# Kernel optimization log

Hardware: AMD Instinct MI355X
Metric: run time of the kernel (lower is better)

Reference implementation:

```python
import jax, jax.numpy as jnp
import numpy as np

DIM = 128
N_CENTERS = 30
CUT_LO, CUT_HI = 0.0, 10.0
N_CONV = 3
NODE_VOCAB = 100
EDGE_VOCAB = 500
N_NODES = 50000
N_EDGES = 800000
N_GRAPHS = 100
DIM_E = DIM + N_CENTERS  # 158


def setup_inputs() -> dict:
    key = jax.random.key(0)
    ks = jax.random.split(key, 20)
    def xav(k, shape):
        fan_in = shape[-2] if len(shape) >= 2 else shape[-1]
        return (jax.random.normal(k, shape, dtype=jnp.float32) / np.sqrt(fan_in)).astype(jnp.float32)
    inp = {
        'node_types': jax.random.randint(ks[0], (N_NODES,), 0, NODE_VOCAB),
        'edge_types': jax.random.randint(ks[1], (N_EDGES,), 0, EDGE_VOCAB),
        'src': jax.random.randint(ks[2], (N_EDGES,), 0, N_NODES),
        'dst': jax.random.randint(ks[3], (N_EDGES,), 0, N_NODES),
        'graph_ids': jnp.sort(jax.random.randint(ks[4], (N_NODES,), 0, N_GRAPHS)),
        'distances': jax.random.uniform(ks[5], (N_EDGES,), dtype=jnp.float32, minval=CUT_LO, maxval=CUT_HI),
        'n_graphs': N_GRAPHS,
        # embedding tables
        'node_emb': xav(ks[6], (NODE_VOCAB, DIM)),
        'edge_emb': xav(ks[7], (EDGE_VOCAB, DIM)),
        # stacked per-conv-layer weights (n_conv leading dim)
        'Wn1': xav(ks[8], (N_CONV, DIM, DIM)),  'bn1': jnp.zeros((N_CONV, DIM), jnp.float32),
        'Wn2': xav(ks[9], (N_CONV, DIM, DIM)),  'bn2': jnp.zeros((N_CONV, DIM), jnp.float32),
        'We1': xav(ks[10], (N_CONV, DIM_E, DIM)), 'be1': jnp.zeros((N_CONV, DIM), jnp.float32),
        'We2': xav(ks[11], (N_CONV, DIM, DIM)),  'be2': jnp.zeros((N_CONV, DIM), jnp.float32),
        'Wc':  xav(ks[12], (N_CONV, DIM, DIM)),  'bc': jnp.zeros((N_CONV, DIM), jnp.float32),
        # read layer
        'Wr1': xav(ks[13], (DIM, DIM)), 'br1': jnp.zeros((DIM,), jnp.float32),
        'Wr2': xav(ks[14], (DIM, 1)),   'br2': jnp.zeros((1,), jnp.float32),
    }
    return inp


def reference(node_types, edge_types, src, dst, graph_ids, distances, n_graphs,
              node_emb, edge_emb, Wn1, bn1, Wn2, bn2, We1, be1, We2, be2, Wc, bc,
              Wr1, br1, Wr2, br2):
    # embeddings
    h = node_emb[node_types]                      # [N, D]
    e_emb = edge_emb[edge_types]                  # [E, D]
    # RBF expansion of distances
    centers = jnp.linspace(CUT_LO, CUT_HI, N_CENTERS, dtype=jnp.float32)
    gap = centers[1] - centers[0]
    rbf = jnp.exp(-((distances[:, None] - centers[None, :]) ** 2) / gap)  # [E, n_centers]
    e = jnp.concatenate([e_emb, rbf], axis=1)     # [E, D + n_centers]

    n_nodes = h.shape[0]
    for i in range(N_CONV):
        node_path = jnp.maximum(h[src] @ Wn1[i] + bn1[i], 0.0) @ Wn2[i] + bn2[i]   # [E, D]
        edge_path = jnp.maximum(e @ We1[i] + be1[i], 0.0) @ We2[i] + be2[i]        # [E, D]
        m = jnp.tanh((node_path * edge_path) @ Wc[i] + bc[i])                       # [E, D]
        h = h + jax.ops.segment_sum(m, dst, num_segments=n_nodes)                   # scatter-add to dst

    # readout MLP + per-graph node sum
    hr = jnp.maximum(h @ Wr1 + br1, 0.0) @ Wr2 + br2                                # [N, 1]
    out = jax.ops.segment_sum(hr, graph_ids, num_segments=n_graphs)                 # [G, 1]
    return out.reshape(-1)
```

## Files before the change

### kernel.cpp

```cpp
#include <hip/hip_runtime.h>
#include <stdint.h>

#define NNODES 50000
#define NEDGES 800000
#define NGRAPH 100
#define NTILES (NEDGES / 128)

typedef _Float16 f16;
typedef __attribute__((ext_vector_type(8))) _Float16 half8;
typedef __attribute__((ext_vector_type(4))) float floatx4;

__device__ __forceinline__ void stage_WT(const float* __restrict__ W, f16* WT,
                                         int tid, int nthr) {
    for (int idx = tid; idx < 128 * 32; idx += nthr) {
        int k = idx >> 5, n4 = (idx & 31) * 4;
        floatx4 v = *(const floatx4*)(W + k * 128 + n4);
        WT[(n4 + 0) * 136 + k] = (f16)v[0];
        WT[(n4 + 1) * 136 + k] = (f16)v[1];
        WT[(n4 + 2) * 136 + k] = (f16)v[2];
        WT[(n4 + 3) * 136 + k] = (f16)v[3];
    }
}

__device__ __forceinline__ float fast_tanh(float x) {
    x = fminf(fmaxf(x, -15.0f), 15.0f);
    float e2 = __expf(2.0f * x);
    return (e2 - 1.0f) * __builtin_amdgcn_rcpf(e2 + 1.0f);
}

__global__ void init_k(float* out, int osz, int* cnt) {
    int i = blockIdx.x * 256 + threadIdx.x;
    if (i < osz) out[i] = 0.0f;
    if (i < NNODES) cnt[i] = 0;
}

__global__ void hist_k(const int* __restrict__ dst, int* __restrict__ cnt) {
    int e = blockIdx.x * 256 + threadIdx.x;
    if (e < NEDGES) atomicAdd(&cnt[dst[e]], 1);
}

__global__ __launch_bounds__(1024) void scan1_k(const int* __restrict__ cnt,
                                                int* __restrict__ rowStart,
                                                int* __restrict__ blockSum) {
    __shared__ int buf[1024];
    int tid = threadIdx.x;
    int i = blockIdx.x * 1024 + tid;
    int v = (i < NNODES) ? cnt[i] : 0;
    buf[tid] = v;
    __syncthreads();
    for (int off = 1; off < 1024; off <<= 1) {
        int t = (tid >= off) ? buf[tid - off] : 0;
        __syncthreads();
        buf[tid] += t;
        __syncthreads();
    }
    if (i < NNODES) rowStart[i] = buf[tid] - v;
    if (tid == 1023) blockSum[blockIdx.x] = buf[1023];
}

__global__ void scan2_k(int* __restrict__ blockSum, int nb) {
    if (threadIdx.x == 0) {
        int run = 0;
        for (int b = 0; b < nb; ++b) { int s = blockSum[b]; blockSum[b] = run; run += s; }
    }
}

__global__ __launch_bounds__(1024) void scan3_k(int* __restrict__ rowStart,
                                                const int* __restrict__ blockSum,
                                                int* __restrict__ cnt) {
    int i = blockIdx.x * 1024 + threadIdx.x;
    if (i < NNODES) { rowStart[i] += blockSum[blockIdx.x]; cnt[i] = 0; }
    if (i == 0) rowStart[NNODES] = NEDGES;
}

__global__ void scatter_k(const int* __restrict__ src, const int* __restrict__ et,
                          const int* __restrict__ dst, const float* __restrict__ dist,
                          const int* __restrict__ rowStart, int* __restrict__ cnt,
                          uint4* __restrict__ packE) {
    int e = blockIdx.x * 256 + threadIdx.x;
    if (e >= NEDGES) return;
    int d = dst[e];
    int pos = rowStart[d] + atomicAdd(&cnt[d], 1);
    uint4 pk;
    pk.x = (unsigned)src[e];
    pk.y = (unsigned)et[e];
    pk.z = (unsigned)d;
    pk.w = __float_as_uint(dist[e]);
    packE[pos] = pk;
}

__global__ void gather_h(const int* __restrict__ nt, const float* __restrict__ emb,
                         float* __restrict__ h) {
    int i = blockIdx.x * 256 + threadIdx.x;
    int row = i >> 5, c4 = (i & 31) * 4;
    if (row < NNODES)
        *(floatx4*)(h + row * 128 + c4) = *(const floatx4*)(emb + nt[row] * 128 + c4);
}

template <int MODE>
__global__ __launch_bounds__(1024, 4) void mlp_kernel(
        const float* __restrict__ X, int M,
        const float* __restrict__ W1, const float* __restrict__ b1,
        const float* __restrict__ W2, const float* __restrict__ b2,
        f16* __restrict__ Out) {
    __shared__ f16 W1T[128 * 136];
    __shared__ f16 W2T[(MODE == 0) ? 128 * 136 : 8];
    __shared__ f16 xBuf[256 * 136];
    __shared__ float bias1[128];
    __shared__ float bias2[128];
    int tid = threadIdx.x;

    stage_WT(W1, W1T, tid, 1024);
    if (MODE == 0) stage_WT(W2, W2T, tid, 1024);
    if (tid < 128) { bias1[tid] = b1[tid]; bias2[tid] = (MODE == 0) ? b2[tid] : 0.0f; }

    int r0 = blockIdx.x * 256;
    for (int it = 0; it < 8; ++it) {
        int row = it * 32 + (tid >> 5);
        int c4 = (tid & 31) * 4;
        int gr = r0 + row;
        floatx4 x = {0.0f, 0.0f, 0.0f, 0.0f};
        if (gr < M) x = *(const floatx4*)(X + (size_t)gr * 128 + c4);
        f16* dph = xBuf + row * 136 + c4;
        dph[0] = (f16)x[0]; dph[1] = (f16)x[1]; dph[2] = (f16)x[2]; dph[3] = (f16)x[3];
    }
    __syncthreads();

    int lane = tid & 63, wv = tid >> 6;
    int R = wv * 16;
    int n16 = lane & 15, q = lane >> 4;

    half8 a[4];
    #pragma unroll
    for (int kk = 0; kk < 4; ++kk)
        a[kk] = *(const half8*)(xBuf + (R + n16) * 136 + kk * 32 + q * 8);

    floatx4 acc[8];
    #pragma unroll
    for (int f = 0; f < 8; ++f) {
        float bb = bias1[f * 16 + n16];
        acc[f] = (floatx4){bb, bb, bb, bb};
        #pragma unroll
        for (int kk = 0; kk < 4; ++kk) {
            half8 b = *(const half8*)(W1T + (f * 16 + n16) * 136 + kk * 32 + q * 8);
            acc[f] = __builtin_amdgcn_mfma_f32_16x16x32_f16(a[kk], b, acc[f], 0, 0, 0);
        }
    }

    if (MODE == 0) {
        #pragma unroll
        for (int f = 0; f < 8; ++f)
            #pragma unroll
            for (int i = 0; i < 4; ++i)
                xBuf[(R + q * 4 + i) * 136 + f * 16 + n16] = (f16)fmaxf(acc[f][i], 0.0f);
        #pragma unroll
        for (int kk = 0; kk < 4; ++kk)
            a[kk] = *(const half8*)(xBuf + (R + n16) * 136 + kk * 32 + q * 8);
        #pragma unroll
        for (int f = 0; f < 8; ++f) {
            float bb = bias2[f * 16 + n16];
            acc[f] = (floatx4){bb, bb, bb, bb};
            #pragma unroll
            for (int kk = 0; kk < 4; ++kk) {
                half8 b = *(const half8*)(W2T + (f * 16 + n16) * 136 + kk * 32 + q * 8);
                acc[f] = __builtin_amdgcn_mfma_f32_16x16x32_f16(a[kk], b, acc[f], 0, 0, 0);
            }
        }
        #pragma unroll
        for (int f = 0; f < 8; ++f)
            #pragma unroll
            for (int i = 0; i < 4; ++i) {
                int gr = r0 + R + q * 4 + i;
                if (gr < M) Out[(size_t)gr * 128 + f * 16 + n16] = (f16)acc[f][i];
            }
    } else {
        #pragma unroll
        for (int f = 0; f < 8; ++f)
            #pragma unroll
            for (int i = 0; i < 4; ++i) {
                int gr = r0 + R + q * 4 + i;
                float v = acc[f][i];
                if (MODE == 1) v = fmaxf(v, 0.0f);
                if (gr < M) Out[(size_t)gr * 128 + f * 16 + n16] = (f16)v;
            }
    }
}

__global__ __launch_bounds__(1024, 4) void edge_kernel(
        const uint4* __restrict__ packE,
        const f16* __restrict__ P, const f16* __restrict__ T,
        const float* __restrict__ We1,
        const float* __restrict__ We2, const float* __restrict__ be2,
        const float* __restrict__ Wc,  const float* __restrict__ bc,
        float* __restrict__ h) {
    __shared__ f16 W2T[128 * 136];
    __shared__ f16 WcT[128 * 136];
    __shared__ f16 W1rT[128 * 40];
    __shared__ f16 uBuf[2][128 * 136];
    __shared__ float sbe2[128], sbc[128];
    __shared__ int   dstSeg[2][128];
    __shared__ int   srcS[2][128];
    __shared__ float distS[2][128];

    int tid = threadIdx.x;
    stage_WT(We2, W2T, tid, 1024);
    stage_WT(Wc,  WcT, tid, 1024);
    for (int idx = tid; idx < 128 * 32; idx += 1024) {
        int n = idx >> 5, kr = idx & 31;
        W1rT[n * 40 + kr] = (kr < 30) ? (f16)We1[(128 + kr) * 128 + n] : (f16)0.0f;
    }
    if (tid < 128) { sbe2[tid] = be2[tid]; sbc[tid] = bc[tid]; }
    __syncthreads();

    int g = tid >> 9;
    int t = tid & 511;
    int lane = tid & 63, wvg = t >> 6;
    int R = wvg * 16;
    int n16 = lane & 15, q = lane >> 4;
    const float invgap = 29.0f / 10.0f;
    f16* U = uBuf[g];

    int gid = blockIdx.x * 2 + g;
    int blkTiles = (NTILES - blockIdx.x * 2 + 511) / 512;

    for (int it = 0; it < blkTiles; ++it) {
        int tile = gid + it * 512;
        bool active = tile < NTILES;

        if (active) {
            int row = t >> 2, sub = t & 3;
            uint4 pk = packE[(size_t)tile * 128 + row];
            if (sub == 0) {
                dstSeg[g][row] = (int)pk.z;
                srcS[g][row]   = (int)pk.x;
                distS[g][row]  = __uint_as_float(pk.w);
            }
            const uint4* Tp = (const uint4*)(T + (size_t)pk.y * 128 + sub * 32);
            uint4* ub = (uint4*)(U + row * 136 + sub * 32);
            ub[0] = Tp[0]; ub[1] = Tp[1]; ub[2] = Tp[2]; ub[3] = Tp[3];
        }

        {
            float d = distS[g][R + n16];
            half8 ar;
            #pragma unroll
            for (int j = 0; j < 8; ++j) {
                int k = q * 8 + j;
                float c = (float)k * (10.0f / 29.0f);
                float df = d - c;
                ar[j] = (f16)((k < 30) ? __expf(-df * df * invgap) : 0.0f);
            }
            #pragma unroll
            for (int f = 0; f < 8; ++f) {
                int col = f * 16 + n16;
                floatx4 c4;
                #pragma unroll
                for (int i = 0; i < 4; ++i) c4[i] = (float)U[(R + q * 4 + i) * 136 + col];
                half8 br = *(const half8*)(W1rT + col * 40 + q * 8);
                c4 = __builtin_amdgcn_mfma_f32_16x16x32_f16(ar, br, c4, 0, 0, 0);
                #pragma unroll
                for (int i = 0; i < 4; ++i)
                    U[(R + q * 4 + i) * 136 + col] = (f16)fmaxf(c4[i], 0.0f);
            }
        }

        half8 pA[4];
        {
            int srow = active ? srcS[g][R + n16] : 0;
            const f16* Pr = P + (size_t)srow * 128 + q * 8;
            #pragma unroll
            for (int kk = 0; kk < 4; ++kk) pA[kk] = *(const half8*)(Pr + kk * 32);
        }

        half8 a2[4];
        #pragma unroll
        for (int kk = 0; kk < 4; ++kk)
            a2[kk] = *(const half8*)(U + (R + n16) * 136 + kk * 32 + q * 8);
        floatx4 ep[8];
        #pragma unroll
        for (int f = 0; f < 8; ++f) {
            float bb = sbe2[f * 16 + n16];
            ep[f] = (floatx4){bb, bb, bb, bb};
            #pragma unroll
            for (int kk = 0; kk < 4; ++kk) {
                half8 b = *(const half8*)(W2T + (f * 16 + n16) * 136 + kk * 32 + q * 8);
                ep[f] = __builtin_amdgcn_mfma_f32_16x16x32_f16(a2[kk], b, ep[f], 0, 0, 0);
            }
        }

        #pragma unroll
        for (int f = 0; f < 8; ++f) {
            int col = f * 16 + n16;
            #pragma unroll
            for (int i = 0; i < 4; ++i)
                U[(R + q * 4 + i) * 136 + col] = (f16)ep[f][i];
        }

        #pragma unroll
        for (int kk = 0; kk < 4; ++kk) {
            half8 pe = *(const half8*)(U + (R + n16) * 136 + kk * 32 + q * 8);
            a2[kk] = pe * pA[kk];
        }
        floatx4 mm[8];
        #pragma unroll
        for (int f = 0; f < 8; ++f) {
            float bb = sbc[f * 16 + n16];
            mm[f] = (floatx4){bb, bb, bb, bb};
            #pragma unroll
            for (int kk = 0; kk < 4; ++kk) {
                half8 b = *(const half8*)(WcT + (f * 16 + n16) * 136 + kk * 32 + q * 8);
                mm[f] = __builtin_amdgcn_mfma_f32_16x16x32_f16(a2[kk], b, mm[f], 0, 0, 0);
            }
        }
        #pragma unroll
        for (int f = 0; f < 8; ++f)
            #pragma unroll
            for (int i = 0; i < 4; ++i)
                U[(R + q * 4 + i) * 136 + f * 16 + n16] = (f16)fast_tanh(mm[f][i]);
        __syncthreads();

        if (active) {
            int col = t & 127, chunk = t >> 7;
            int rbeg = chunk * 32;
            float acc = 0.0f;
            int prev = dstSeg[g][rbeg];
            for (int r = rbeg; r < rbeg + 32; ++r) {
                int dd = dstSeg[g][r];
                float v = (float)U[r * 136 + col];
                if (dd != prev) {
                    unsafeAtomicAdd(&h[(size_t)prev * 128 + col], acc);
                    acc = v; prev = dd;
                } else acc += v;
            }
            unsafeAtomicAdd(&h[(size_t)prev * 128 + col], acc);
        }
        __syncthreads();
    }
}

__global__ void dot_k(const f16* __restrict__ tbuf, const float* __restrict__ Wr2,
                      const float* __restrict__ br2, const int* __restrict__ gid,
                      float* __restrict__ out) {
    __shared__ float sa[256];
    __shared__ int sg[256];
    int t = threadIdx.x;
    int n = blockIdx.x * 256 + t;
    float acc = 0.0f;
    int g = -1;
    if (n < NNODES) {
        const half8* tp = (const half8*)(tbuf + (size_t)n * 128);
        for (int m = 0; m < 16; ++m) {
            half8 v = tp[m];
            for (int j = 0; j < 8; ++j) acc += (float)v[j] * Wr2[m * 8 + j];
        }
        acc += br2[0];
        g = gid[n];
    }
    sa[t] = acc; sg[t] = g;
    __syncthreads();
    if (n < NNODES) {
        bool head = (t == 0) || (sg[t - 1] != g);
        if (head) {
            float s = 0.0f;
            int r = t;
            while (r < 256 && sg[r] == g) { s += sa[r]; ++r; }
            unsafeAtomicAdd(&out[g], s);
        }
    }
}

extern "C" void kernel_launch(void* const* d_in, const int* in_sizes, int n_in,
                              void* d_out, int out_size, void* d_ws, size_t ws_size,
                              hipStream_t stream) {
    (void)in_sizes; (void)n_in; (void)ws_size;
    const int*   node_types = (const int*)d_in[0];
    const int*   edge_types = (const int*)d_in[1];
    const int*   src        = (const int*)d_in[2];
    const int*   dst        = (const int*)d_in[3];
    const int*   graph_ids  = (const int*)d_in[4];
    const float* distances  = (const float*)d_in[5];
    const float* node_emb   = (const float*)d_in[7];
    const float* edge_emb   = (const float*)d_in[8];
    const float* Wn1 = (const float*)d_in[9];
    const float* bn1 = (const float*)d_in[10];
    const float* Wn2 = (const float*)d_in[11];
    const float* bn2 = (const float*)d_in[12];
    const float* We1 = (const float*)d_in[13];
    const float* be1 = (const float*)d_in[14];
    const float* We2 = (const float*)d_in[15];
    const float* be2 = (const float*)d_in[16];
    const float* Wc  = (const float*)d_in[17];
    const float* bc  = (const float*)d_in[18];
    const float* Wr1 = (const float*)d_in[19];
    const float* br1 = (const float*)d_in[20];
    const float* Wr2 = (const float*)d_in[21];
    const float* br2 = (const float*)d_in[22];

    char* w = (char*)d_ws;
    auto carve = [&](size_t bytes) { char* p = w; w += (bytes + 255) & ~(size_t)255; return p; };
    float* h        = (float*)carve((size_t)NNODES * 128 * 4);
    f16*   P        = (f16*)  carve((size_t)NNODES * 128 * 2);
    f16*   T        = (f16*)  carve((size_t)500 * 128 * 2);
    int*   rowStart = (int*)  carve((size_t)(NNODES + 1) * 4);
    int*   cnt      = (int*)  carve((size_t)NNODES * 4);
    int*   blockSum = (int*)  carve((size_t)64 * 4);
    uint4* packE    = (uint4*)carve((size_t)NEDGES * 16);

    float* out = (float*)d_out;
    const int NB1 = (NNODES + 1023) / 1024;

    init_k<<<(NNODES + 255) / 256, 256, 0, stream>>>(out, out_size, cnt);
    hist_k<<<NEDGES / 256, 256, 0, stream>>>(dst, cnt);
    scan1_k<<<NB1, 1024, 0, stream>>>(cnt, rowStart, blockSum);
    scan2_k<<<1, 64, 0, stream>>>(blockSum, NB1);
    scan3_k<<<NB1, 1024, 0, stream>>>(rowStart, blockSum, cnt);
    scatter_k<<<NEDGES / 256, 256, 0, stream>>>(src, edge_types, dst, distances,
                                                rowStart, cnt, packE);
    gather_h<<<(NNODES * 32 + 255) / 256, 256, 0, stream>>>(node_types, node_emb, h);

    for (int i = 0; i < 3; ++i) {
        mlp_kernel<2><<<(500 + 255) / 256, 1024, 0, stream>>>(
            edge_emb, 500, We1 + (size_t)i * 158 * 128, be1 + i * 128, nullptr, nullptr, T);
        mlp_kernel<0><<<(NNODES + 255) / 256, 1024, 0, stream>>>(
            h, NNODES, Wn1 + (size_t)i * 128 * 128, bn1 + i * 128,
            Wn2 + (size_t)i * 128 * 128, bn2 + i * 128, P);
        edge_kernel<<<256, 1024, 0, stream>>>(
            packE, P, T,
            We1 + (size_t)i * 158 * 128,
            We2 + (size_t)i * 128 * 128, be2 + i * 128,
            Wc + (size_t)i * 128 * 128, bc + i * 128, h);
    }

    mlp_kernel<1><<<(NNODES + 255) / 256, 1024, 0, stream>>>(
        h, NNODES, Wr1, br1, nullptr, nullptr, P);
    dot_k<<<(NNODES + 255) / 256, 256, 0, stream>>>(P, Wr2, br2, graph_ids, out);
}
```

Before: 827.4 us.

## Make edge kernel wave-independent with carried segment sums and fuse readout

```diff
diff --git a/kernel.cpp b/kernel.cpp
--- a/kernel.cpp
+++ b/kernel.cpp
@@ -4,10 +4,12 @@
 #define NNODES 50000
 #define NEDGES 800000
 #define NGRAPH 100
-#define NTILES (NEDGES / 128)
+#define NCHUNK (NEDGES / 16)
+#define NWAVES 4096
 
 typedef _Float16 f16;
 typedef __attribute__((ext_vector_type(8))) _Float16 half8;
+typedef __attribute__((ext_vector_type(4))) _Float16 half4;
 typedef __attribute__((ext_vector_type(4))) float floatx4;
 
 __device__ __forceinline__ void stage_WT(const float* __restrict__ W, f16* WT,
@@ -26,6 +28,10 @@
     x = fminf(fmaxf(x, -15.0f), 15.0f);
     float e2 = __expf(2.0f * x);
     return (e2 - 1.0f) * __builtin_amdgcn_rcpf(e2 + 1.0f);
+}
+
+__device__ __forceinline__ int mtAddr(int c, int rgroup) {
+    return c * 16 + ((((c >> 2) + rgroup) & 3) << 2);
 }
 
 __global__ void init_k(float* out, int osz, int* cnt) {
@@ -179,9 +185,7 @@
             #pragma unroll
             for (int i = 0; i < 4; ++i) {
                 int gr = r0 + R + q * 4 + i;
-                float v = acc[f][i];
-                if (MODE == 1) v = fmaxf(v, 0.0f);
-                if (gr < M) Out[(size_t)gr * 128 + f * 16 + n16] = (f16)v;
+                if (gr < M) Out[(size_t)gr * 128 + f * 16 + n16] = (f16)acc[f][i];
             }
     }
 }
@@ -196,11 +200,9 @@
     __shared__ f16 W2T[128 * 136];
     __shared__ f16 WcT[128 * 136];
     __shared__ f16 W1rT[128 * 40];
-    __shared__ f16 uBuf[2][128 * 136];
+    __shared__ f16 Uall[16 * 2176];
     __shared__ float sbe2[128], sbc[128];
-    __shared__ int   dstSeg[2][128];
-    __shared__ int   srcS[2][128];
-    __shared__ float distS[2][128];
+    __shared__ int dstW[16][16];
 
     int tid = threadIdx.x;
     stage_WT(We2, W2T, tid, 1024);
@@ -212,36 +214,43 @@
     if (tid < 128) { sbe2[tid] = be2[tid]; sbc[tid] = bc[tid]; }
     __syncthreads();
 
-    int g = tid >> 9;
-    int t = tid & 511;
-    int lane = tid & 63, wvg = t >> 6;
-    int R = wvg * 16;
+    int lane = tid & 63, wv = tid >> 6;
+    f16* U = Uall + wv * 2176;
+    int* dW = dstW[wv];
     int n16 = lane & 15, q = lane >> 4;
     const float invgap = 29.0f / 10.0f;
-    f16* U = uBuf[g];
-
-    int gid = blockIdx.x * 2 + g;
-    int blkTiles = (NTILES - blockIdx.x * 2 + 511) / 512;
-
-    for (int it = 0; it < blkTiles; ++it) {
-        int tile = gid + it * 512;
-        bool active = tile < NTILES;
-
-        if (active) {
-            int row = t >> 2, sub = t & 3;
-            uint4 pk = packE[(size_t)tile * 128 + row];
-            if (sub == 0) {
-                dstSeg[g][row] = (int)pk.z;
-                srcS[g][row]   = (int)pk.x;
-                distS[g][row]  = __uint_as_float(pk.w);
-            }
-            const uint4* Tp = (const uint4*)(T + (size_t)pk.y * 128 + sub * 32);
+    int colA = lane, colB = lane + 64;
+
+    int wgid = blockIdx.x * 16 + wv;
+    const int CPW = (NCHUNK + NWAVES - 1) / NWAVES;
+    int c0 = wgid * CPW;
+    int c1 = c0 + CPW; if (c1 > NCHUNK) c1 = NCHUNK;
+
+    float carry0 = 0.0f, carry1 = 0.0f;
+    int prev = -1;
+
+    for (int ch = c0; ch < c1; ++ch) {
+        int e0 = ch * 16;
+        uint4 pk = {0u, 0u, 0u, 0u};
+        if (lane < 16) pk = packE[e0 + lane];
+        int   ety  = __shfl((int)pk.y, lane >> 2);
+        int   srcv = __shfl((int)pk.x, n16);
+        float d    = __shfl(__uint_as_float(pk.w), n16);
+        if (lane < 16) dW[lane] = (int)pk.z;
+        {
+            int row = lane >> 2, sub = lane & 3;
+            const uint4* Tp = (const uint4*)(T + (size_t)ety * 128 + sub * 32);
             uint4* ub = (uint4*)(U + row * 136 + sub * 32);
             ub[0] = Tp[0]; ub[1] = Tp[1]; ub[2] = Tp[2]; ub[3] = Tp[3];
         }
-
+        half8 pA[4];
         {
-            float d = distS[g][R + n16];
+            const f16* Pr = P + (size_t)srcv * 128 + q * 8;
+            #pragma unroll
+            for (int kk = 0; kk < 4; ++kk) pA[kk] = *(const half8*)(Pr + kk * 32);
+        }
+
+        {
             half8 ar;
             #pragma unroll
             for (int j = 0; j < 8; ++j) {
@@ -255,27 +264,19 @@
                 int col = f * 16 + n16;
                 floatx4 c4;
                 #pragma unroll
-                for (int i = 0; i < 4; ++i) c4[i] = (float)U[(R + q * 4 + i) * 136 + col];
+                for (int i = 0; i < 4; ++i) c4[i] = (float)U[(q * 4 + i) * 136 + col];
                 half8 br = *(const half8*)(W1rT + col * 40 + q * 8);
                 c4 = __builtin_amdgcn_mfma_f32_16x16x32_f16(ar, br, c4, 0, 0, 0);
                 #pragma unroll
                 for (int i = 0; i < 4; ++i)
-                    U[(R + q * 4 + i) * 136 + col] = (f16)fmaxf(c4[i], 0.0f);
-            }
-        }
-
-        half8 pA[4];
-        {
-            int srow = active ? srcS[g][R + n16] : 0;
-            const f16* Pr = P + (size_t)srow * 128 + q * 8;
-            #pragma unroll
-            for (int kk = 0; kk < 4; ++kk) pA[kk] = *(const half8*)(Pr + kk * 32);
+                    U[(q * 4 + i) * 136 + col] = (f16)fmaxf(c4[i], 0.0f);
+            }
         }
 
         half8 a2[4];
         #pragma unroll
         for (int kk = 0; kk < 4; ++kk)
-            a2[kk] = *(const half8*)(U + (R + n16) * 136 + kk * 32 + q * 8);
+            a2[kk] = *(const half8*)(U + n16 * 136 + kk * 32 + q * 8);
         floatx4 ep[8];
         #pragma unroll
         for (int f = 0; f < 8; ++f) {
@@ -293,12 +294,12 @@
             int col = f * 16 + n16;
             #pragma unroll
             for (int i = 0; i < 4; ++i)
-                U[(R + q * 4 + i) * 136 + col] = (f16)ep[f][i];
+                U[(q * 4 + i) * 136 + col] = (f16)ep[f][i];
         }
 
         #pragma unroll
         for (int kk = 0; kk < 4; ++kk) {
-            half8 pe = *(const half8*)(U + (R + n16) * 136 + kk * 32 + q * 8);
+            half8 pe = *(const half8*)(U + n16 * 136 + kk * 32 + q * 8);
             a2[kk] = pe * pA[kk];
         }
         floatx4 mm[8];
@@ -313,59 +314,120 @@
             }
         }
         #pragma unroll
+        for (int f = 0; f < 8; ++f) {
+            int c = f * 16 + n16;
+            half4 mv;
+            #pragma unroll
+            for (int i = 0; i < 4; ++i) mv[i] = (f16)fast_tanh(mm[f][i]);
+            *(half4*)(U + mtAddr(c, q)) = mv;
+        }
+
+        {
+            half4 va[4], vb[4];
+            #pragma unroll
+            for (int g2 = 0; g2 < 4; ++g2) {
+                va[g2] = *(const half4*)(U + mtAddr(colA, g2));
+                vb[g2] = *(const half4*)(U + mtAddr(colB, g2));
+            }
+            int dArr[16];
+            *(int4*)(dArr)      = *(const int4*)(dW);
+            *(int4*)(dArr + 4)  = *(const int4*)(dW + 4);
+            *(int4*)(dArr + 8)  = *(const int4*)(dW + 8);
+            *(int4*)(dArr + 12) = *(const int4*)(dW + 12);
+            #pragma unroll
+            for (int r = 0; r < 16; ++r) {
+                int dd = dArr[r];
+                float v0 = (float)va[r >> 2][r & 3];
+                float v1 = (float)vb[r >> 2][r & 3];
+                if (dd != prev) {
+                    if (prev >= 0) {
+                        unsafeAtomicAdd(&h[(size_t)prev * 128 + colA], carry0);
+                        unsafeAtomicAdd(&h[(size_t)prev * 128 + colB], carry1);
+                    }
+                    prev = dd; carry0 = v0; carry1 = v1;
+                } else { carry0 += v0; carry1 += v1; }
+            }
+        }
+    }
+    if (prev >= 0) {
+        unsafeAtomicAdd(&h[(size_t)prev * 128 + colA], carry0);
+        unsafeAtomicAdd(&h[(size_t)prev * 128 + colB], carry1);
+    }
+}
+
+__global__ __launch_bounds__(1024, 4) void readout_k(
+        const float* __restrict__ X, int M,
+        const float* __restrict__ W1, const float* __restrict__ b1,
+        const float* __restrict__ Wr2, const float* __restrict__ br2,
+        const int* __restrict__ gid, float* __restrict__ out) {
+    __shared__ f16 W1T[128 * 136];
+    __shared__ f16 xBuf[256 * 136];
+    __shared__ float bias1[128];
+    __shared__ float sWr2[128];
+    int tid = threadIdx.x;
+
+    stage_WT(W1, W1T, tid, 1024);
+    if (tid < 128) { bias1[tid] = b1[tid]; sWr2[tid] = Wr2[tid]; }
+
+    int r0 = blockIdx.x * 256;
+    for (int it = 0; it < 8; ++it) {
+        int row = it * 32 + (tid >> 5);
+        int c4 = (tid & 31) * 4;
+        int gr = r0 + row;
+        floatx4 x = {0.0f, 0.0f, 0.0f, 0.0f};
+        if (gr < M) x = *(const floatx4*)(X + (size_t)gr * 128 + c4);
+        f16* dph = xBuf + row * 136 + c4;
+        dph[0] = (f16)x[0]; dph[1] = (f16)x[1]; dph[2] = (f16)x[2]; dph[3] = (f16)x[3];
+    }
+    __syncthreads();
+
+    int lane = tid & 63, wv = tid >> 6;
+    int R = wv * 16;
+    int n16 = lane & 15, q = lane >> 4;
+
+    half8 a[4];
+    #pragma unroll
+    for (int kk = 0; kk < 4; ++kk)
+        a[kk] = *(const half8*)(xBuf + (R + n16) * 136 + kk * 32 + q * 8);
+
+    floatx4 acc[8];
+    #pragma unroll
+    for (int f = 0; f < 8; ++f) {
+        float bb = bias1[f * 16 + n16];
+        acc[f] = (floatx4){bb, bb, bb, bb};
+        #pragma unroll
+        for (int kk = 0; kk < 4; ++kk) {
+            half8 b = *(const half8*)(W1T + (f * 16 + n16) * 136 + kk * 32 + q * 8);
+            acc[f] = __builtin_amdgcn_mfma_f32_16x16x32_f16(a[kk], b, acc[f], 0, 0, 0);
+        }
+    }
+
+    float s[4];
+    #pragma unroll
+    for (int i = 0; i < 4; ++i) {
+        float t = 0.0f;
+        #pragma unroll
         for (int f = 0; f < 8; ++f)
-            #pragma unroll
-            for (int i = 0; i < 4; ++i)
-                U[(R + q * 4 + i) * 136 + f * 16 + n16] = (f16)fast_tanh(mm[f][i]);
-        __syncthreads();
-
-        if (active) {
-            int col = t & 127, chunk = t >> 7;
-            int rbeg = chunk * 32;
-            float acc = 0.0f;
-            int prev = dstSeg[g][rbeg];
-            for (int r = rbeg; r < rbeg + 32; ++r) {
-                int dd = dstSeg[g][r];
-                float v = (float)U[r * 136 + col];
-                if (dd != prev) {
-                    unsafeAtomicAdd(&h[(size_t)prev * 128 + col], acc);
-                    acc = v; prev = dd;
-                } else acc += v;
-            }
-            unsafeAtomicAdd(&h[(size_t)prev * 128 + col], acc);
-        }
-        __syncthreads();
-    }
-}
-
-__global__ void dot_k(const f16* __restrict__ tbuf, const float* __restrict__ Wr2,
-                      const float* __restrict__ br2, const int* __restrict__ gid,
-                      float* __restrict__ out) {
-    __shared__ float sa[256];
-    __shared__ int sg[256];
-    int t = threadIdx.x;
-    int n = blockIdx.x * 256 + t;
-    float acc = 0.0f;
-    int g = -1;
-    if (n < NNODES) {
-        const half8* tp = (const half8*)(tbuf + (size_t)n * 128);
-        for (int m = 0; m < 16; ++m) {
-            half8 v = tp[m];
-            for (int j = 0; j < 8; ++j) acc += (float)v[j] * Wr2[m * 8 + j];
-        }
-        acc += br2[0];
-        g = gid[n];
-    }
-    sa[t] = acc; sg[t] = g;
-    __syncthreads();
-    if (n < NNODES) {
-        bool head = (t == 0) || (sg[t - 1] != g);
-        if (head) {
-            float s = 0.0f;
-            int r = t;
-            while (r < 256 && sg[r] == g) { s += sa[r]; ++r; }
-            unsafeAtomicAdd(&out[g], s);
-        }
+            t += fmaxf(acc[f][i], 0.0f) * sWr2[f * 16 + n16];
+        #pragma unroll
+        for (int m = 1; m < 16; m <<= 1) t += __shfl_xor(t, m);
+        s[i] = t;
+    }
+
+    if (n16 == 0) {
+        float br2v = br2[0];
+        float t = 0.0f; int g = -1;
+        #pragma unroll
+        for (int i = 0; i < 4; ++i) {
+            int gr = r0 + R + q * 4 + i;
+            if (gr < M) {
+                int gi = gid[gr];
+                float si = s[i] + br2v;
+                if (gi == g) t += si;
+                else { if (g >= 0) unsafeAtomicAdd(&out[g], t); g = gi; t = si; }
+            }
+        }
+        if (g >= 0) unsafeAtomicAdd(&out[g], t);
     }
 }
 
@@ -431,7 +493,6 @@
             Wc + (size_t)i * 128 * 128, bc + i * 128, h);
     }
 
-    mlp_kernel<1><<<(NNODES + 255) / 256, 1024, 0, stream>>>(
-        h, NNODES, Wr1, br1, nullptr, nullptr, P);
-    dot_k<<<(NNODES + 255) / 256, 256, 0, stream>>>(P, Wr2, br2, graph_ids, out);
-}
+    readout_k<<<(NNODES + 255) / 256, 1024, 0, stream>>>(
+        h, NNODES, Wr1, br1, Wr2, br2, graph_ids, out);
+}
```

New measurement: 735.6 us, median of 2. 11.1% less time.
